# Performance work log

Measured on AMD Instinct MI355X. Metric: run time of the kernel, lower is better.

The kernel has to match this reference:

```python
import jax, jax.numpy as jnp
import numpy as np
from jax.scipy.linalg import solve_triangular

B, T, D = 2, 8192, 1024
HEAD_DIM = 128
H = D // HEAD_DIM  # 8 heads
C = 64             # chunk size (hard-coded in the torch module)


def setup_inputs() -> dict:
    key = jax.random.key(0)
    k0, k1, k2, k3 = jax.random.split(key, 4)
    scale = 0.02
    return {
        "out": jax.random.normal(k0, (B, T, D), jnp.float32),
        "W_write": jax.random.normal(k1, (D, D), jnp.float32) * scale,   # proj_write.weight (out,in)
        "W_read": jax.random.normal(k2, (D, D), jnp.float32) * scale,    # proj_read.weight
        "W_beta": jax.random.normal(k3, (H, D), jnp.float32) * scale,    # proj_beta.weight
        "decay": jnp.full((H,), 4.6, jnp.float32),                        # decay parameter
    }


def reference(out, W_write, W_read, W_beta, decay):
    Bs, Ts, Ds = out.shape
    d = HEAD_DIM
    Hn = Ds // d
    x = out.astype(jnp.float32)

    # keys: L2-normalized per head (F.normalize, eps=1e-12)
    k = x.reshape(Bs, Ts, Hn, d)
    k = k / jnp.maximum(jnp.linalg.norm(k, axis=-1, keepdims=True), 1e-12)
    k = k.transpose(0, 2, 1, 3)                                   # (B,H,T,d)
    v = (x @ W_write.T).reshape(Bs, Ts, Hn, d).transpose(0, 2, 1, 3)
    beta = jax.nn.sigmoid(x @ W_beta.T).transpose(0, 2, 1)[..., None]  # (B,H,T,1)
    v = v * beta
    k_beta = k * beta

    pad = (-Ts) % C
    if pad:
        pw = ((0, 0), (0, 0), (0, pad), (0, 0))
        k, v, k_beta = (jnp.pad(a, pw) for a in (k, v, k_beta))
    Tp = k.shape[2]
    N = Tp // C

    log_gamma = jnp.log(jax.nn.sigmoid(decay))                     # (H,)
    pos = jnp.arange(C, dtype=jnp.float32)
    cum_decay = (pos + 1.0)[None, :] * log_gamma[:, None]          # (H,C)
    Ldiff = cum_decay[:, :, None] - cum_decay[:, None, :]
    L = jnp.tril(jnp.exp(jnp.tril(Ldiff)))                         # (H,C,C)
    decay_exp = jnp.exp(cum_decay)[None, :, None, :, None]         # (1,H,1,C,1)
    chunk_total_decay = jnp.exp(cum_decay[:, -1])[None, :, None, None]  # (1,H,1,1)
    dw = jnp.exp(cum_decay[:, -1:] - cum_decay)[None, :, :, None]  # (1,H,C,1)
    de = jnp.exp(cum_decay)[None, :, :, None]                      # (1,H,C,1)

    k = k.reshape(Bs, Hn, N, C, d)
    v = v.reshape(Bs, Hn, N, C, d)
    k_beta = k_beta.reshape(Bs, Hn, N, C, d)

    # UT transform: original loop computes A = (I - A0)^{-1} with A0 strictly lower
    A0 = jnp.tril(-(jnp.einsum('bhnid,bhnjd->bhnij', k_beta, k) * L[None, :, None]), -1)
    eye = jnp.eye(C, dtype=jnp.float32)
    M = eye - A0                                                    # unit-diag lower triangular
    A = solve_triangular(M, jnp.broadcast_to(eye, M.shape), lower=True, unit_diagonal=True)

    v = A @ v
    k_cumdecay = A @ (k_beta * decay_exp)

    # inter-chunk sequential recurrence over N chunks
    kc = k.transpose(2, 0, 1, 3, 4)            # (N,B,H,C,d)
    vc = v.transpose(2, 0, 1, 3, 4)
    kcd = k_cumdecay.transpose(2, 0, 1, 3, 4)

    def step(S, inp):
        k_i, v_i, kcd_i = inp                  # (B,H,C,d)
        attn = jnp.tril(jnp.einsum('bhid,bhjd->bhij', k_i, k_i) * L[None])
        v_new = v_i - kcd_i @ S
        o_i = (k_i * de) @ S + attn @ v_new
        S_new = chunk_total_decay * S + jnp.einsum('bhcd,bhce->bhde', k_i * dw, v_new)
        return S_new, o_i

    S0 = jnp.zeros((Bs, Hn, d, d), jnp.float32)
    _, o = jax.lax.scan(step, S0, (kc, vc, kcd))  # o: (N,B,H,C,d)

    o = o.transpose(1, 2, 0, 3, 4).reshape(Bs, Hn, Tp, d)
    o = o.transpose(0, 2, 1, 3).reshape(Bs, Tp, Ds)[:, :Ts]
    return out + (o @ W_read.T).astype(out.dtype)
```

## Files before the change

kernel.cpp:

```cpp
#include <hip/hip_runtime.h>
#include <stdint.h>

#define DEV static __device__ __forceinline__

typedef float          f32x4  __attribute__((ext_vector_type(4)));
typedef short          bf16x8 __attribute__((ext_vector_type(8)));
typedef unsigned short u16x4  __attribute__((ext_vector_type(4)));
typedef unsigned short u16x8  __attribute__((ext_vector_type(8)));

#define B_   2
#define T_   8192
#define D_   1024
#define H_   8
#define HD_  128
#define N_   128

DEV float dot4(const float4& a, const float4& b) {
    return a.x * b.x + a.y * b.y + a.z * b.z + a.w * b.w;
}
DEV unsigned short f2bf(float f) {
    union { float f; unsigned u; } v; v.f = f;
    unsigned r = (v.u + 0x7fffu + ((v.u >> 16) & 1u)) >> 16;
    return (unsigned short)r;
}
DEV float bf2f(unsigned short u) {
    union { unsigned u; float f; } v; v.u = ((unsigned)u) << 16;
    return v.f;
}
DEV unsigned pk2(unsigned short h, unsigned short l) {
    return (unsigned)h | ((unsigned)l << 16);
}
DEV bf16x8 mk8(unsigned a, unsigned b, unsigned c, unsigned d) {
    union { unsigned u[4]; bf16x8 v; } t;
    t.u[0] = a; t.u[1] = b; t.u[2] = c; t.u[3] = d;
    return t.v;
}
DEV void cvt4(const float4 v, u16x4* h, u16x4* l) {
    const float* p = (const float*)&v;
    #pragma unroll
    for (int i = 0; i < 4; ++i) {
        unsigned short hv = f2bf(p[i]);
        (*h)[i] = hv;
        (*l)[i] = f2bf(p[i] - bf2f(hv));
    }
}
DEV int swzu(int c, int u) { return u ^ (((c & 7) << 2) | ((c >> 3) & 3)); }

DEV float4* r512(char* base, int r, int u) {
    return (float4*)(base + (r << 9) + ((u << 4) ^ ((r & 7) << 4)));
}

__launch_bounds__(256)
__global__ void prep_kernel(const float* __restrict__ X, const float* __restrict__ Wb,
                            unsigned short* __restrict__ khi, unsigned short* __restrict__ klo,
                            float* __restrict__ beta) {
    int bt = blockIdx.x;
    int b = bt >> 13, t = bt & 8191;
    __shared__ float xrow[D_];
    const float* xp = X + (size_t)bt * D_;
    for (int i = threadIdx.x; i < D_; i += 256) xrow[i] = xp[i];
    __syncthreads();
    int w = threadIdx.x >> 6, lane = threadIdx.x & 63;
    for (int h = w; h < H_; h += 4) {
        const float* xh = xrow + h * HD_;
        float a0 = xh[lane], a1 = xh[lane + 64];
        float s = a0 * a0 + a1 * a1;
        #pragma unroll
        for (int off = 32; off > 0; off >>= 1) s += __shfl_xor(s, off);
        float rn = 1.0f / fmaxf(sqrtf(s), 1e-12f);
        const float* wbh = Wb + (size_t)h * D_;
        float bs = 0.f;
        for (int i = lane; i < D_; i += 64) bs += xrow[i] * wbh[i];
        #pragma unroll
        for (int off = 32; off > 0; off >>= 1) bs += __shfl_xor(bs, off);
        float bet = 1.0f / (1.0f + expf(-bs));
        size_t kbase = ((size_t)(b * H_ + h) * T_ + t) * HD_;
        float x0 = a0 * rn, x1 = a1 * rn;
        unsigned short h0 = f2bf(x0), h1 = f2bf(x1);
        khi[kbase + lane]      = h0;
        khi[kbase + lane + 64] = h1;
        klo[kbase + lane]      = f2bf(x0 - bf2f(h0));
        klo[kbase + lane + 64] = f2bf(x1 - bf2f(h1));
        if (lane == 0) beta[(size_t)(b * H_ + h) * T_ + t] = bet;
    }
}

__launch_bounds__(256, 2)
__global__ void vproj_kernel(const float* __restrict__ X, const float* __restrict__ W,
                             const float* __restrict__ beta, float* __restrict__ vb) {
    extern __shared__ char gs[];
    char* AH = gs;
    char* AL = gs + 16384;
    char* BH = gs + 32768;
    char* BL = gs + 49152;
    int bm = blockIdx.x, bn = blockIdx.y;
    int tid = threadIdx.x;
    int w = tid >> 6, lr = tid & 15, lk = (tid & 63) >> 4;
    int wm = w >> 1, wn = w & 1;

    f32x4 acc[4][4];
    #pragma unroll
    for (int i = 0; i < 4; ++i)
        #pragma unroll
        for (int j = 0; j < 4; ++j) acc[i][j] = (f32x4){0.f, 0.f, 0.f, 0.f};

    for (int kt = 0; kt < 16; ++kt) {
        __syncthreads();
        #pragma unroll
        for (int q = 0; q < 8; ++q) {
            int f = tid + q * 256;
            int row = f >> 4, kq = f & 15;
            float4 av = *(const float4*)(X + (size_t)(bm * 128 + row) * D_ + kt * 64 + kq * 4);
            float4 bv = *(const float4*)(W + (size_t)(bn * 128 + row) * D_ + kt * 64 + kq * 4);
            u16x4 ah, al, bh, bl;
            cvt4(av, &ah, &al);
            cvt4(bv, &bh, &bl);
            int off = row * 128 + ((((kq >> 1) ^ (row & 7))) << 4) + ((kq & 1) << 3);
            *(u16x4*)(AH + off) = ah; *(u16x4*)(AL + off) = al;
            *(u16x4*)(BH + off) = bh; *(u16x4*)(BL + off) = bl;
        }
        __syncthreads();
        #pragma unroll
        for (int ks = 0; ks < 2; ++ks) {
            bf16x8 aH[4], aL[4], bH[4], bL[4];
            #pragma unroll
            for (int mt = 0; mt < 4; ++mt) {
                int row = wm * 64 + mt * 16 + lr;
                int off = row * 128 + (((ks * 4 + lk) ^ (row & 7)) << 4);
                aH[mt] = *(const bf16x8*)(AH + off);
                aL[mt] = *(const bf16x8*)(AL + off);
            }
            #pragma unroll
            for (int nt = 0; nt < 4; ++nt) {
                int row = wn * 64 + nt * 16 + lr;
                int off = row * 128 + (((ks * 4 + lk) ^ (row & 7)) << 4);
                bH[nt] = *(const bf16x8*)(BH + off);
                bL[nt] = *(const bf16x8*)(BL + off);
            }
            #pragma unroll
            for (int mt = 0; mt < 4; ++mt)
                #pragma unroll
                for (int nt = 0; nt < 4; ++nt) {
                    acc[mt][nt] = __builtin_amdgcn_mfma_f32_16x16x32_bf16(aH[mt], bH[nt], acc[mt][nt], 0, 0, 0);
                    acc[mt][nt] = __builtin_amdgcn_mfma_f32_16x16x32_bf16(aH[mt], bL[nt], acc[mt][nt], 0, 0, 0);
                    acc[mt][nt] = __builtin_amdgcn_mfma_f32_16x16x32_bf16(aL[mt], bH[nt], acc[mt][nt], 0, 0, 0);
                }
        }
    }
    #pragma unroll
    for (int mt = 0; mt < 4; ++mt)
        #pragma unroll
        for (int r = 0; r < 4; ++r) {
            int m = bm * 128 + wm * 64 + mt * 16 + lk * 4 + r;
            int b = m >> 13, t = m & 8191;
            float bet = beta[(size_t)(b * H_ + bn) * T_ + t];
            size_t ob = ((size_t)(b * H_ + bn) * T_ + t) * HD_;
            #pragma unroll
            for (int nt = 0; nt < 4; ++nt)
                vb[ob + wn * 64 + nt * 16 + lr] = acc[mt][nt][r] * bet;
        }
}

__launch_bounds__(256, 2)
__global__ void chunk_kernel(const unsigned short* __restrict__ khi,
                             const unsigned short* __restrict__ klo,
                             float* __restrict__ vb,
                             const float* __restrict__ beta_g,
                             const float* __restrict__ decay,
                             unsigned short* __restrict__ attn_g,
                             unsigned short* __restrict__ kcdhi_g,
                             unsigned short* __restrict__ kcdlo_g) {
    extern __shared__ char cs[];
    char*  sk = cs;
    float* sa = (float*)(cs + 32768);
    float* sm = (float*)(cs + 49152);
    __shared__ float sb[64];
    __shared__ float swgt[64];

    int cid = blockIdx.x;
    int bh = cid >> 7, cn = cid & 127;
    int h = bh & 7;
    int tid = threadIdx.x;
    float dec = decay[h];
    float sg = 1.0f / (1.0f + expf(-dec));
    float lg = logf(sg);
    size_t base = (size_t)cid * 8192;

    #pragma unroll
    for (int lq = 0; lq < 4; ++lq) {
        int f = tid + lq * 256;
        int c = f >> 4, u0 = (f & 15) << 1;
        u16x8 hh = *(const u16x8*)(khi + base + (size_t)f * 8);
        u16x8 ll = *(const u16x8*)(klo + base + (size_t)f * 8);
        float4 v0 = {bf2f(hh[0]) + bf2f(ll[0]), bf2f(hh[1]) + bf2f(ll[1]),
                     bf2f(hh[2]) + bf2f(ll[2]), bf2f(hh[3]) + bf2f(ll[3])};
        float4 v1 = {bf2f(hh[4]) + bf2f(ll[4]), bf2f(hh[5]) + bf2f(ll[5]),
                     bf2f(hh[6]) + bf2f(ll[6]), bf2f(hh[7]) + bf2f(ll[7])};
        *r512(sk, c, u0)     = v0;
        *r512(sk, c, u0 + 1) = v1;
    }
    if (tid < 64) {
        float bv = beta_g[(size_t)bh * T_ + cn * 64 + tid];
        sb[tid] = bv;
        swgt[tid] = bv * expf((float)(tid + 1) * lg);
    }
    __syncthreads();

    int bi = tid >> 4, bj = tid & 15;
    float dacc[4][4] = {};
    for (int u = 0; u < 32; ++u) {
        float4 ka[4], kc[4];
        #pragma unroll
        for (int i = 0; i < 4; ++i) ka[i] = *r512(sk, bi * 4 + i, u);
        #pragma unroll
        for (int j = 0; j < 4; ++j) kc[j] = *r512(sk, bj + 16 * j, u);
        #pragma unroll
        for (int i = 0; i < 4; ++i)
            #pragma unroll
            for (int j = 0; j < 4; ++j)
                dacc[i][j] += dot4(ka[i], kc[j]);
    }
    size_t abase = (size_t)cid * 4096;
    #pragma unroll
    for (int i = 0; i < 4; ++i) {
        int gi = bi * 4 + i;
        #pragma unroll
        for (int j = 0; j < 4; ++j) {
            int gj = bj + 16 * j;
            float dv = dacc[i][j];
            float dfac = expf((float)(gi - gj) * lg);
            attn_g[abase + (size_t)gi * 64 + gj] = (gi >= gj) ? f2bf(dv * dfac) : (unsigned short)0;
            sm[gi * 64 + gj] = (gj < gi) ? sb[gi] * dv * dfac : ((gi == gj) ? 1.f : 0.f);
        }
    }
    __syncthreads();

    if (tid < 64) {
        int j = tid;
        for (int i = 0; i < j; ++i) sa[i * 64 + j] = 0.f;
        sa[j * 64 + j] = 1.f;
        for (int i = j + 1; i < 64; ++i) {
            float s = 0.f;
            for (int p = j; p < i; ++p) s += sm[i * 64 + p] * sa[p * 64 + j];
            sa[i * 64 + j] = -s;
        }
    }
    __syncthreads();

    int ti = tid >> 4, te = tid & 15;
    {
        float ko[4][8] = {};
        for (int p = 0; p < 64; ++p) {
            float w = swgt[p];
            float4 k0 = *r512(sk, p, te * 2);
            float4 k1 = *r512(sk, p, te * 2 + 1);
            float kv[8] = {k0.x, k0.y, k0.z, k0.w, k1.x, k1.y, k1.z, k1.w};
            float a0 = sa[(ti * 4 + 0) * 64 + p] * w;
            float a1 = sa[(ti * 4 + 1) * 64 + p] * w;
            float a2 = sa[(ti * 4 + 2) * 64 + p] * w;
            float a3 = sa[(ti * 4 + 3) * 64 + p] * w;
            #pragma unroll
            for (int e = 0; e < 8; ++e) {
                ko[0][e] = fmaf(a0, kv[e], ko[0][e]);
                ko[1][e] = fmaf(a1, kv[e], ko[1][e]);
                ko[2][e] = fmaf(a2, kv[e], ko[2][e]);
                ko[3][e] = fmaf(a3, kv[e], ko[3][e]);
            }
        }
        #pragma unroll
        for (int i = 0; i < 4; ++i) {
            u16x8 hh, ll;
            #pragma unroll
            for (int e = 0; e < 8; ++e) {
                float t = -ko[i][e];
                unsigned short hv = f2bf(t);
                hh[e] = hv;
                ll[e] = f2bf(t - bf2f(hv));
            }
            size_t off = base + (size_t)(ti * 4 + i) * 128 + te * 8;
            *(u16x8*)(kcdhi_g + off) = hh;
            *(u16x8*)(kcdlo_g + off) = ll;
        }
    }
    __syncthreads();

    #pragma unroll
    for (int lq = 0; lq < 8; ++lq) {
        int f = tid + lq * 256;
        int r = f >> 5, u = f & 31;
        *r512(sk, r, u) = ((const float4*)(vb + base))[f];
    }
    __syncthreads();

    {
        float vo[4][8] = {};
        for (int p = 0; p < 64; ++p) {
            float4 v0 = *r512(sk, p, te * 2);
            float4 v1 = *r512(sk, p, te * 2 + 1);
            float vv[8] = {v0.x, v0.y, v0.z, v0.w, v1.x, v1.y, v1.z, v1.w};
            float a0 = sa[(ti * 4 + 0) * 64 + p];
            float a1 = sa[(ti * 4 + 1) * 64 + p];
            float a2 = sa[(ti * 4 + 2) * 64 + p];
            float a3 = sa[(ti * 4 + 3) * 64 + p];
            #pragma unroll
            for (int e = 0; e < 8; ++e) {
                vo[0][e] = fmaf(a0, vv[e], vo[0][e]);
                vo[1][e] = fmaf(a1, vv[e], vo[1][e]);
                vo[2][e] = fmaf(a2, vv[e], vo[2][e]);
                vo[3][e] = fmaf(a3, vv[e], vo[3][e]);
            }
        }
        #pragma unroll
        for (int i = 0; i < 4; ++i) {
            float4 lo = {vo[i][0], vo[i][1], vo[i][2], vo[i][3]};
            float4 hi = {vo[i][4], vo[i][5], vo[i][6], vo[i][7]};
            size_t off = base + (size_t)(ti * 4 + i) * 128 + te * 8;
            *(float4*)(vb + off)     = lo;
            *(float4*)(vb + off + 4) = hi;
        }
    }
}

__launch_bounds__(512, 1)
__global__ void scan_kernel(const unsigned short* __restrict__ khi,
                            const unsigned short* __restrict__ klo,
                            const float* __restrict__ vpr,
                            const unsigned short* __restrict__ kcdhi,
                            const unsigned short* __restrict__ kcdlo,
                            const unsigned short* __restrict__ att,
                            const float* __restrict__ decay,
                            unsigned short* __restrict__ obuf) {
    extern __shared__ char ls[];
    char* KP = ls;
    char* SH = ls + 65536;
    char* SL = ls + 69632;
    char* VH = ls + 73728;
    char* VL = ls + 75776;
    char* WH = ls + 77824;
    char* WL = ls + 79872;

    int bid = blockIdx.x;
    int h7 = bid & 7;
    int strip = (bid >> 3) & 7;
    int bh = ((bid >> 6) << 3) + h7;
    int e0 = strip * 16;
    int tid = threadIdx.x;
    int w = tid >> 6, l = tid & 63, lr = l & 15, lk = l >> 4;
    int grp = w >> 2, cw = w & 3;
    float dec = decay[bh & 7];
    float sg = 1.0f / (1.0f + expf(-dec));
    float lg = logf(sg);
    float g64 = expf(64.f * lg);
    float dev4[4], gw4[4];
    #pragma unroll
    for (int r = 0; r < 4; ++r) {
        int c = cw * 16 + lk * 4 + r;
        dev4[r] = expf((float)(c + 1) * lg);
        gw4[r]  = expf((float)(63 - c) * lg);
    }

    f32x4 Sacc = (f32x4){0.f, 0.f, 0.f, 0.f};

    unsigned sh_[4][4], sl_[4][4];
    bf16x8 fH[4], fL[4];
    bf16x8 atA[2];
    f32x4 vnA;

    {
        size_t nb = (size_t)bh * N_ * 8192;
        size_t na = (size_t)bh * N_ * 4096;
        #pragma unroll
        for (int q = 0; q < 4; ++q) {
            int idx = tid + q * 512;
            u16x4 hh = *(const u16x4*)(khi + nb + (size_t)idx * 4);
            u16x4 ll = *(const u16x4*)(klo + nb + (size_t)idx * 4);
            #pragma unroll
            for (int j = 0; j < 4; ++j) { sh_[q][j] = hh[j]; sl_[q][j] = ll[j]; }
        }
        if (grp == 0) {
            #pragma unroll
            for (int ks = 0; ks < 4; ++ks) {
                size_t off = nb + (size_t)(cw * 16 + lr) * 128 + ks * 32 + lk * 8;
                fH[ks] = *(const bf16x8*)(kcdhi + off);
                fL[ks] = *(const bf16x8*)(kcdlo + off);
            }
            #pragma unroll
            for (int r = 0; r < 4; ++r)
                vnA[r] = vpr[nb + (size_t)(cw * 16 + lk * 4 + r) * 128 + e0 + lr];
        } else {
            #pragma unroll
            for (int ks = 0; ks < 4; ++ks) {
                size_t off = nb + (size_t)(cw * 16 + lr) * 128 + ks * 32 + lk * 8;
                fH[ks] = *(const bf16x8*)(khi + off);
                fL[ks] = *(const bf16x8*)(klo + off);
            }
            #pragma unroll
            for (int ks2 = 0; ks2 < 2; ++ks2)
                atA[ks2] = *(const bf16x8*)(att + na + (size_t)(cw * 16 + lr) * 64 + ks2 * 32 + lk * 8);
        }
        #pragma unroll
        for (int q = 0; q < 4; ++q) {
            int idx = tid + q * 512;
            int c = idx >> 5, un = idx & 31;
            uint4 pkd = {pk2((unsigned short)sh_[q][0], (unsigned short)sl_[q][0]),
                         pk2((unsigned short)sh_[q][1], (unsigned short)sl_[q][1]),
                         pk2((unsigned short)sh_[q][2], (unsigned short)sl_[q][2]),
                         pk2((unsigned short)sh_[q][3], (unsigned short)sl_[q][3])};
            *(uint4*)(KP + c * 512 + (swzu(c, un) << 4)) = pkd;
        }
    }

    for (int cn = 0; cn < N_; ++cn) {
        const char* KPc = KP + (cn & 1) * 32768;

        {
            u16x4 h4, l4;
            #pragma unroll
            for (int r = 0; r < 4; ++r) {
                unsigned short hv = f2bf(Sacc[r]);
                h4[r] = hv;
                l4[r] = f2bf(Sacc[r] - bf2f(hv));
            }
            int unit = 2 * w + (lk >> 1);
            int off = lr * 256 + ((unit ^ (lr & 7)) << 4) + ((lk & 1) << 3);
            *(u16x4*)(SH + off) = h4;
            *(u16x4*)(SL + off) = l4;
        }
        __syncthreads();

        bf16x8 BH[4], BL[4];
        #pragma unroll
        for (int ks = 0; ks < 4; ++ks) {
            int off = lr * 256 + (((ks * 4 + lk) ^ (lr & 7)) << 4);
            BH[ks] = *(const bf16x8*)(SH + off);
            BL[ks] = *(const bf16x8*)(SL + off);
        }
        f32x4 acc1, acc2;
        if (grp == 0) {
            acc1 = vnA; acc2 = (f32x4){0.f, 0.f, 0.f, 0.f};
            __builtin_amdgcn_s_setprio(1);
            #pragma unroll
            for (int ks = 0; ks < 2; ++ks) {
                acc1 = __builtin_amdgcn_mfma_f32_16x16x32_bf16(fH[ks], BH[ks], acc1, 0, 0, 0);
                acc2 = __builtin_amdgcn_mfma_f32_16x16x32_bf16(fH[ks+2], BH[ks+2], acc2, 0, 0, 0);
                acc1 = __builtin_amdgcn_mfma_f32_16x16x32_bf16(fH[ks], BL[ks], acc1, 0, 0, 0);
                acc2 = __builtin_amdgcn_mfma_f32_16x16x32_bf16(fH[ks+2], BL[ks+2], acc2, 0, 0, 0);
                acc1 = __builtin_amdgcn_mfma_f32_16x16x32_bf16(fL[ks], BH[ks], acc1, 0, 0, 0);
                acc2 = __builtin_amdgcn_mfma_f32_16x16x32_bf16(fL[ks+2], BH[ks+2], acc2, 0, 0, 0);
            }
            __builtin_amdgcn_s_setprio(0);
            u16x4 h4, l4, wh4, wl4;
            #pragma unroll
            for (int r = 0; r < 4; ++r) {
                float vv = acc1[r] + acc2[r];
                unsigned short hv = f2bf(vv);
                h4[r] = hv; l4[r] = f2bf(vv - bf2f(hv));
                float wv = vv * gw4[r];
                unsigned short wh = f2bf(wv);
                wh4[r] = wh; wl4[r] = f2bf(wv - bf2f(wh));
            }
            int cu = 2 * cw + (lk >> 1);
            int off = lr * 128 + ((cu ^ (lr & 7)) << 4) + ((lk & 1) << 3);
            *(u16x4*)(VH + off) = h4;  *(u16x4*)(VL + off) = l4;
            *(u16x4*)(WH + off) = wh4; *(u16x4*)(WL + off) = wl4;
        } else {
            acc1 = (f32x4){0.f, 0.f, 0.f, 0.f}; acc2 = acc1;
            __builtin_amdgcn_s_setprio(1);
            #pragma unroll
            for (int ks = 0; ks < 2; ++ks) {
                acc1 = __builtin_amdgcn_mfma_f32_16x16x32_bf16(fH[ks], BH[ks], acc1, 0, 0, 0);
                acc2 = __builtin_amdgcn_mfma_f32_16x16x32_bf16(fH[ks+2], BH[ks+2], acc2, 0, 0, 0);
                acc1 = __builtin_amdgcn_mfma_f32_16x16x32_bf16(fH[ks], BL[ks], acc1, 0, 0, 0);
                acc2 = __builtin_amdgcn_mfma_f32_16x16x32_bf16(fH[ks+2], BL[ks+2], acc2, 0, 0, 0);
                acc1 = __builtin_amdgcn_mfma_f32_16x16x32_bf16(fL[ks], BH[ks], acc1, 0, 0, 0);
                acc2 = __builtin_amdgcn_mfma_f32_16x16x32_bf16(fL[ks+2], BH[ks+2], acc2, 0, 0, 0);
            }
            __builtin_amdgcn_s_setprio(0);
        }
        __syncthreads();

        bf16x8 WHf[2], WLf[2];
        #pragma unroll
        for (int ks2 = 0; ks2 < 2; ++ks2) {
            int off = lr * 128 + (((ks2 * 4 + lk) ^ (lr & 7)) << 4);
            WHf[ks2] = *(const bf16x8*)(WH + off);
            WLf[ks2] = *(const bf16x8*)(WL + off);
        }
        if (grp == 1) {
            bf16x8 VHf[2], VLf[2];
            #pragma unroll
            for (int ks2 = 0; ks2 < 2; ++ks2) {
                int off = lr * 128 + (((ks2 * 4 + lk) ^ (lr & 7)) << 4);
                VHf[ks2] = *(const bf16x8*)(VH + off);
                VLf[ks2] = *(const bf16x8*)(VL + off);
            }
            f32x4 om;
            #pragma unroll
            for (int r = 0; r < 4; ++r) om[r] = (acc1[r] + acc2[r]) * dev4[r];
            #pragma unroll
            for (int ks2 = 0; ks2 < 2; ++ks2) {
                om = __builtin_amdgcn_mfma_f32_16x16x32_bf16(atA[ks2], VHf[ks2], om, 0, 0, 0);
                om = __builtin_amdgcn_mfma_f32_16x16x32_bf16(atA[ks2], VLf[ks2], om, 0, 0, 0);
            }
            size_t ob = ((size_t)bh * T_ + (size_t)cn * 64) * 128 + e0 + lr;
            #pragma unroll
            for (int r = 0; r < 4; ++r)
                obuf[ob + (size_t)(cw * 16 + lk * 4 + r) * 128] = f2bf(om[r]);
        }

        if (cn + 1 < N_) {
            size_t nb = ((size_t)bh * N_ + cn + 1) * 8192;
            size_t na = ((size_t)bh * N_ + cn + 1) * 4096;
            #pragma unroll
            for (int q = 0; q < 4; ++q) {
                int idx = tid + q * 512;
                u16x4 hh = *(const u16x4*)(khi + nb + (size_t)idx * 4);
                u16x4 ll = *(const u16x4*)(klo + nb + (size_t)idx * 4);
                #pragma unroll
                for (int j = 0; j < 4; ++j) { sh_[q][j] = hh[j]; sl_[q][j] = ll[j]; }
            }
            if (grp == 0) {
                #pragma unroll
                for (int ks = 0; ks < 4; ++ks) {
                    size_t off = nb + (size_t)(cw * 16 + lr) * 128 + ks * 32 + lk * 8;
                    fH[ks] = *(const bf16x8*)(kcdhi + off);
                    fL[ks] = *(const bf16x8*)(kcdlo + off);
                }
                #pragma unroll
                for (int r = 0; r < 4; ++r)
                    vnA[r] = vpr[nb + (size_t)(cw * 16 + lk * 4 + r) * 128 + e0 + lr];
            } else {
                #pragma unroll
                for (int ks = 0; ks < 4; ++ks) {
                    size_t off = nb + (size_t)(cw * 16 + lr) * 128 + ks * 32 + lk * 8;
                    fH[ks] = *(const bf16x8*)(khi + off);
                    fL[ks] = *(const bf16x8*)(klo + off);
                }
                #pragma unroll
                for (int ks2 = 0; ks2 < 2; ++ks2)
                    atA[ks2] = *(const bf16x8*)(att + na + (size_t)(cw * 16 + lr) * 64 + ks2 * 32 + lk * 8);
            }
        }

        {
            #pragma unroll
            for (int r = 0; r < 4; ++r) Sacc[r] *= g64;
            int dk = w * 16 + lr;
            int du = dk >> 2, db = (dk & 3) << 2;
            bf16x8 tH[2], tL[2];
            #pragma unroll
            for (int ks2 = 0; ks2 < 2; ++ks2) {
                unsigned uv[8];
                #pragma unroll
                for (int j = 0; j < 8; ++j) {
                    int c = ks2 * 32 + lk * 8 + j;
                    uv[j] = *(const unsigned*)(KPc + c * 512 + (swzu(c, du) << 4) + db);
                }
                tH[ks2] = mk8((uv[0] & 0xffffu) | (uv[1] << 16), (uv[2] & 0xffffu) | (uv[3] << 16),
                              (uv[4] & 0xffffu) | (uv[5] << 16), (uv[6] & 0xffffu) | (uv[7] << 16));
                tL[ks2] = mk8((uv[0] >> 16) | (uv[1] & 0xffff0000u), (uv[2] >> 16) | (uv[3] & 0xffff0000u),
                              (uv[4] >> 16) | (uv[5] & 0xffff0000u), (uv[6] >> 16) | (uv[7] & 0xffff0000u));
            }
            f32x4 tmp = (f32x4){0.f, 0.f, 0.f, 0.f};
            __builtin_amdgcn_s_setprio(1);
            Sacc = __builtin_amdgcn_mfma_f32_16x16x32_bf16(tH[0], WHf[0], Sacc, 0, 0, 0);
            tmp  = __builtin_amdgcn_mfma_f32_16x16x32_bf16(tH[1], WHf[1], tmp,  0, 0, 0);
            Sacc = __builtin_amdgcn_mfma_f32_16x16x32_bf16(tH[0], WLf[0], Sacc, 0, 0, 0);
            tmp  = __builtin_amdgcn_mfma_f32_16x16x32_bf16(tH[1], WLf[1], tmp,  0, 0, 0);
            Sacc = __builtin_amdgcn_mfma_f32_16x16x32_bf16(tL[0], WHf[0], Sacc, 0, 0, 0);
            tmp  = __builtin_amdgcn_mfma_f32_16x16x32_bf16(tL[1], WHf[1], tmp,  0, 0, 0);
            __builtin_amdgcn_s_setprio(0);
            #pragma unroll
            for (int r = 0; r < 4; ++r) Sacc[r] += tmp[r];
        }

        if (cn + 1 < N_) {
            char* KPn = KP + ((cn + 1) & 1) * 32768;
            #pragma unroll
            for (int q = 0; q < 4; ++q) {
                int idx = tid + q * 512;
                int c = idx >> 5, un = idx & 31;
                uint4 pkd = {pk2((unsigned short)sh_[q][0], (unsigned short)sl_[q][0]),
                             pk2((unsigned short)sh_[q][1], (unsigned short)sl_[q][1]),
                             pk2((unsigned short)sh_[q][2], (unsigned short)sl_[q][2]),
                             pk2((unsigned short)sh_[q][3], (unsigned short)sl_[q][3])};
                *(uint4*)(KPn + c * 512 + (swzu(c, un) << 4)) = pkd;
            }
        }
    }
}

__launch_bounds__(256, 2)
__global__ void final_kernel(const float* __restrict__ X, const float* __restrict__ W,
                             const unsigned short* __restrict__ OB, float* __restrict__ out) {
    extern __shared__ char gs[];
    char* AO = gs;
    char* BH = gs + 16384;
    char* BL = gs + 32768;
    int bm = blockIdx.x, bn = blockIdx.y;
    int tid = threadIdx.x;
    int w = tid >> 6, lr = tid & 15, lk = (tid & 63) >> 4;
    int wm = w >> 1, wn = w & 1;

    f32x4 acc[4][4];
    #pragma unroll
    for (int i = 0; i < 4; ++i)
        #pragma unroll
        for (int j = 0; j < 4; ++j) acc[i][j] = (f32x4){0.f, 0.f, 0.f, 0.f};

    for (int kt = 0; kt < 16; ++kt) {
        int hh = kt >> 1, e0g = (kt & 1) * 64;
        __syncthreads();
        #pragma unroll
        for (int q = 0; q < 4; ++q) {
            int f = tid + q * 256;
            int row = f >> 3, un = f & 7;
            int m = bm * 128 + row;
            int b = m >> 13, t = m & 8191;
            u16x8 av = *(const u16x8*)(OB + (((size_t)(b * H_ + hh) * T_ + t) << 7) + e0g + un * 8);
            int off = row * 128 + ((un ^ (row & 7)) << 4);
            *(u16x8*)(AO + off) = av;
        }
        #pragma unroll
        for (int q = 0; q < 8; ++q) {
            int f = tid + q * 256;
            int row = f >> 4, kq = f & 15;
            float4 bv = *(const float4*)(W + (size_t)(bn * 128 + row) * D_ + kt * 64 + kq * 4);
            u16x4 bh, bl;
            cvt4(bv, &bh, &bl);
            int off = row * 128 + ((((kq >> 1) ^ (row & 7))) << 4) + ((kq & 1) << 3);
            *(u16x4*)(BH + off) = bh; *(u16x4*)(BL + off) = bl;
        }
        __syncthreads();
        #pragma unroll
        for (int ks = 0; ks < 2; ++ks) {
            bf16x8 aO[4], bH[4], bL[4];
            #pragma unroll
            for (int mt = 0; mt < 4; ++mt) {
                int row = wm * 64 + mt * 16 + lr;
                int off = row * 128 + (((ks * 4 + lk) ^ (row & 7)) << 4);
                aO[mt] = *(const bf16x8*)(AO + off);
            }
            #pragma unroll
            for (int nt = 0; nt < 4; ++nt) {
                int row = wn * 64 + nt * 16 + lr;
                int off = row * 128 + (((ks * 4 + lk) ^ (row & 7)) << 4);
                bH[nt] = *(const bf16x8*)(BH + off);
                bL[nt] = *(const bf16x8*)(BL + off);
            }
            #pragma unroll
            for (int mt = 0; mt < 4; ++mt)
                #pragma unroll
                for (int nt = 0; nt < 4; ++nt) {
                    acc[mt][nt] = __builtin_amdgcn_mfma_f32_16x16x32_bf16(aO[mt], bH[nt], acc[mt][nt], 0, 0, 0);
                    acc[mt][nt] = __builtin_amdgcn_mfma_f32_16x16x32_bf16(aO[mt], bL[nt], acc[mt][nt], 0, 0, 0);
                }
        }
    }
    #pragma unroll
    for (int mt = 0; mt < 4; ++mt)
        #pragma unroll
        for (int r = 0; r < 4; ++r) {
            int m = bm * 128 + wm * 64 + mt * 16 + lk * 4 + r;
            size_t xo = (size_t)m * D_ + bn * 128;
            #pragma unroll
            for (int nt = 0; nt < 4; ++nt) {
                int n = wn * 64 + nt * 16 + lr;
                out[xo + n] = X[xo + n] + acc[mt][nt][r];
            }
        }
}

extern "C" void kernel_launch(void* const* d_in, const int* in_sizes, int n_in,
                              void* d_out, int out_size, void* d_ws, size_t ws_size,
                              hipStream_t stream) {
    const float* X   = (const float*)d_in[0];
    const float* Ww  = (const float*)d_in[1];
    const float* Wr  = (const float*)d_in[2];
    const float* Wb  = (const float*)d_in[3];
    const float* dec = (const float*)d_in[4];

    char* ws = (char*)d_ws;
    unsigned short* khi  = (unsigned short*)(ws);
    unsigned short* klo  = (unsigned short*)(ws + 33554432);
    float*          vb   = (float*)(ws + 67108864);
    unsigned short* kcdh = (unsigned short*)(ws + 134217728);
    unsigned short* kcdl = (unsigned short*)(ws + 167772160);
    unsigned short* attn = (unsigned short*)(ws + 201326592);
    float*          beta = (float*)(ws + 218103808);
    unsigned short* obuf = (unsigned short*)(ws + 218628096);
    if (ws_size < 252182528ull) return;

    hipFuncSetAttribute((const void*)vproj_kernel, hipFuncAttributeMaxDynamicSharedMemorySize, 65536);
    hipFuncSetAttribute((const void*)chunk_kernel, hipFuncAttributeMaxDynamicSharedMemorySize, 65536);
    hipFuncSetAttribute((const void*)scan_kernel,  hipFuncAttributeMaxDynamicSharedMemorySize, 81920);
    hipFuncSetAttribute((const void*)final_kernel, hipFuncAttributeMaxDynamicSharedMemorySize, 49152);

    hipLaunchKernelGGL(prep_kernel, dim3(B_ * T_), dim3(256), 0, stream, X, Wb, khi, klo, beta);
    hipLaunchKernelGGL(vproj_kernel, dim3(128, 8), dim3(256), 65536, stream, X, Ww, beta, vb);
    hipLaunchKernelGGL(chunk_kernel, dim3(B_ * H_ * N_), dim3(256), 65536, stream,
                       khi, klo, vb, beta, dec, attn, kcdh, kcdl);
    hipLaunchKernelGGL(scan_kernel, dim3(128), dim3(512), 81920, stream,
                       khi, klo, vb, kcdh, kcdl, attn, dec, obuf);
    hipLaunchKernelGGL(final_kernel, dim3(128, 8), dim3(256), 49152, stream, X, Wr, obuf, (float*)d_out);
}
```

Before: 1.152 ms.

## Precompute decay-weighted transposed keys in chunk kernel, simplify scan state update

The chunk kernel now writes a transposed, decay-weighted copy of k (k*dw) as bf16 hi/lo split, so the sequential scan loads it directly instead of staging k into LDS each step and transposing it. The scan no longer forms a decay-weighted v and uses plain v_new for the state update. Its output is written in fp32 into the v buffer, and the final projection splits it into hi/lo bf16 with an extra MFMA. The lo part of the new buffer, and its MFMA in the state update, are used only when the workspace is large enough; otherwise state-update precision drops. The change adds chunk-kernel work and memory traffic to shorten the serial critical path in the scan.

```diff
diff --git a/kernel.cpp b/kernel.cpp
--- a/kernel.cpp
+++ b/kernel.cpp
@@ -27,14 +27,6 @@
     union { unsigned u; float f; } v; v.u = ((unsigned)u) << 16;
     return v.f;
 }
-DEV unsigned pk2(unsigned short h, unsigned short l) {
-    return (unsigned)h | ((unsigned)l << 16);
-}
-DEV bf16x8 mk8(unsigned a, unsigned b, unsigned c, unsigned d) {
-    union { unsigned u[4]; bf16x8 v; } t;
-    t.u[0] = a; t.u[1] = b; t.u[2] = c; t.u[3] = d;
-    return t.v;
-}
 DEV void cvt4(const float4 v, u16x4* h, u16x4* l) {
     const float* p = (const float*)&v;
     #pragma unroll
@@ -44,10 +36,11 @@
         (*l)[i] = f2bf(p[i] - bf2f(hv));
     }
 }
-DEV int swzu(int c, int u) { return u ^ (((c & 7) << 2) | ((c >> 3) & 3)); }
-
 DEV float4* r512(char* base, int r, int u) {
     return (float4*)(base + (r << 9) + ((u << 4) ^ ((r & 7) << 4)));
+}
+DEV float ld_sk(char* base, int c, int dk) {
+    return *(float*)(base + (c << 9) + ((((dk >> 2) << 4) ^ ((c & 7) << 4)) + ((dk & 3) << 2)));
 }
 
 __launch_bounds__(256)
@@ -169,7 +162,9 @@
                              const float* __restrict__ decay,
                              unsigned short* __restrict__ attn_g,
                              unsigned short* __restrict__ kcdhi_g,
-                             unsigned short* __restrict__ kcdlo_g) {
+                             unsigned short* __restrict__ kcdlo_g,
+                             unsigned short* __restrict__ kdwh_g,
+                             unsigned short* __restrict__ kdwl_g) {
     extern __shared__ char cs[];
     char*  sk = cs;
     float* sa = (float*)(cs + 32768);
@@ -282,6 +277,25 @@
             *(u16x8*)(kcdlo_g + off) = ll;
         }
     }
+
+    {
+        int dk = tid >> 1, ch = (tid & 1) * 32;
+        #pragma unroll
+        for (int q = 0; q < 4; ++q) {
+            u16x8 th, tl;
+            #pragma unroll
+            for (int j = 0; j < 8; ++j) {
+                int c = ch + q * 8 + j;
+                float kv = ld_sk(sk, c, dk) * expf((float)(63 - c) * lg);
+                unsigned short hv = f2bf(kv);
+                th[j] = hv;
+                tl[j] = f2bf(kv - bf2f(hv));
+            }
+            size_t off = base + (size_t)dk * 64 + ch + q * 8;
+            *(u16x8*)(kdwh_g + off) = th;
+            if (kdwl_g) *(u16x8*)(kdwl_g + off) = tl;
+        }
+    }
     __syncthreads();
 
     #pragma unroll
@@ -324,25 +338,21 @@
 __launch_bounds__(512, 1)
 __global__ void scan_kernel(const unsigned short* __restrict__ khi,
                             const unsigned short* __restrict__ klo,
-                            const float* __restrict__ vpr,
-                            const unsigned short* __restrict__ kcdhi,
-                            const unsigned short* __restrict__ kcdlo,
+                            float* __restrict__ vb,
+                            const unsigned short* __restrict__ kcdh,
+                            const unsigned short* __restrict__ kcdl,
                             const unsigned short* __restrict__ att,
-                            const float* __restrict__ decay,
-                            unsigned short* __restrict__ obuf) {
-    extern __shared__ char ls[];
-    char* KP = ls;
-    char* SH = ls + 65536;
-    char* SL = ls + 69632;
-    char* VH = ls + 73728;
-    char* VL = ls + 75776;
-    char* WH = ls + 77824;
-    char* WL = ls + 79872;
+                            const unsigned short* __restrict__ kdwh,
+                            const unsigned short* __restrict__ kdwl,
+                            const float* __restrict__ decay) {
+    __shared__ char SH[4096];
+    __shared__ char SL[4096];
+    __shared__ char VH[2048];
+    __shared__ char VL[2048];
 
     int bid = blockIdx.x;
-    int h7 = bid & 7;
+    int bh = ((bid >> 6) << 3) + (bid & 7);
     int strip = (bid >> 3) & 7;
-    int bh = ((bid >> 6) << 3) + h7;
     int e0 = strip * 16;
     int tid = threadIdx.x;
     int w = tid >> 6, l = tid & 63, lr = l & 15, lk = l >> 4;
@@ -351,17 +361,14 @@
     float sg = 1.0f / (1.0f + expf(-dec));
     float lg = logf(sg);
     float g64 = expf(64.f * lg);
-    float dev4[4], gw4[4];
-    #pragma unroll
-    for (int r = 0; r < 4; ++r) {
-        int c = cw * 16 + lk * 4 + r;
-        dev4[r] = expf((float)(c + 1) * lg);
-        gw4[r]  = expf((float)(63 - c) * lg);
-    }
+    float dev4[4];
+    #pragma unroll
+    for (int r = 0; r < 4; ++r)
+        dev4[r] = expf((float)(cw * 16 + lk * 4 + r + 1) * lg);
+    const bool haveLo = (kdwl != nullptr);
 
     f32x4 Sacc = (f32x4){0.f, 0.f, 0.f, 0.f};
 
-    unsigned sh_[4][4], sl_[4][4];
     bf16x8 fH[4], fL[4];
     bf16x8 atA[2];
     f32x4 vnA;
@@ -369,24 +376,16 @@
     {
         size_t nb = (size_t)bh * N_ * 8192;
         size_t na = (size_t)bh * N_ * 4096;
-        #pragma unroll
-        for (int q = 0; q < 4; ++q) {
-            int idx = tid + q * 512;
-            u16x4 hh = *(const u16x4*)(khi + nb + (size_t)idx * 4);
-            u16x4 ll = *(const u16x4*)(klo + nb + (size_t)idx * 4);
-            #pragma unroll
-            for (int j = 0; j < 4; ++j) { sh_[q][j] = hh[j]; sl_[q][j] = ll[j]; }
-        }
         if (grp == 0) {
             #pragma unroll
             for (int ks = 0; ks < 4; ++ks) {
                 size_t off = nb + (size_t)(cw * 16 + lr) * 128 + ks * 32 + lk * 8;
-                fH[ks] = *(const bf16x8*)(kcdhi + off);
-                fL[ks] = *(const bf16x8*)(kcdlo + off);
+                fH[ks] = *(const bf16x8*)(kcdh + off);
+                fL[ks] = *(const bf16x8*)(kcdl + off);
             }
             #pragma unroll
             for (int r = 0; r < 4; ++r)
-                vnA[r] = vpr[nb + (size_t)(cw * 16 + lk * 4 + r) * 128 + e0 + lr];
+                vnA[r] = vb[nb + (size_t)(cw * 16 + lk * 4 + r) * 128 + e0 + lr];
         } else {
             #pragma unroll
             for (int ks = 0; ks < 4; ++ks) {
@@ -398,20 +397,10 @@
             for (int ks2 = 0; ks2 < 2; ++ks2)
                 atA[ks2] = *(const bf16x8*)(att + na + (size_t)(cw * 16 + lr) * 64 + ks2 * 32 + lk * 8);
         }
-        #pragma unroll
-        for (int q = 0; q < 4; ++q) {
-            int idx = tid + q * 512;
-            int c = idx >> 5, un = idx & 31;
-            uint4 pkd = {pk2((unsigned short)sh_[q][0], (unsigned short)sl_[q][0]),
-                         pk2((unsigned short)sh_[q][1], (unsigned short)sl_[q][1]),
-                         pk2((unsigned short)sh_[q][2], (unsigned short)sl_[q][2]),
-                         pk2((unsigned short)sh_[q][3], (unsigned short)sl_[q][3])};
-            *(uint4*)(KP + c * 512 + (swzu(c, un) << 4)) = pkd;
-        }
     }
 
     for (int cn = 0; cn < N_; ++cn) {
-        const char* KPc = KP + (cn & 1) * 32768;
+        size_t cb8 = ((size_t)bh * N_ + cn) * 8192;
 
         {
             u16x4 h4, l4;
@@ -449,20 +438,16 @@
                 acc2 = __builtin_amdgcn_mfma_f32_16x16x32_bf16(fL[ks+2], BH[ks+2], acc2, 0, 0, 0);
             }
             __builtin_amdgcn_s_setprio(0);
-            u16x4 h4, l4, wh4, wl4;
+            u16x4 h4, l4;
             #pragma unroll
             for (int r = 0; r < 4; ++r) {
                 float vv = acc1[r] + acc2[r];
                 unsigned short hv = f2bf(vv);
                 h4[r] = hv; l4[r] = f2bf(vv - bf2f(hv));
-                float wv = vv * gw4[r];
-                unsigned short wh = f2bf(wv);
-                wh4[r] = wh; wl4[r] = f2bf(wv - bf2f(wh));
             }
             int cu = 2 * cw + (lk >> 1);
             int off = lr * 128 + ((cu ^ (lr & 7)) << 4) + ((lk & 1) << 3);
             *(u16x4*)(VH + off) = h4;  *(u16x4*)(VL + off) = l4;
-            *(u16x4*)(WH + off) = wh4; *(u16x4*)(WL + off) = wl4;
         } else {
             acc1 = (f32x4){0.f, 0.f, 0.f, 0.f}; acc2 = acc1;
             __builtin_amdgcn_s_setprio(1);
@@ -479,21 +464,21 @@
         }
         __syncthreads();
 
-        bf16x8 WHf[2], WLf[2];
+        bf16x8 VHf[2], VLf[2];
         #pragma unroll
         for (int ks2 = 0; ks2 < 2; ++ks2) {
             int off = lr * 128 + (((ks2 * 4 + lk) ^ (lr & 7)) << 4);
-            WHf[ks2] = *(const bf16x8*)(WH + off);
-            WLf[ks2] = *(const bf16x8*)(WL + off);
+            VHf[ks2] = *(const bf16x8*)(VH + off);
+            VLf[ks2] = *(const bf16x8*)(VL + off);
+        }
+        bf16x8 tH[2], tL[2];
+        #pragma unroll
+        for (int ks2 = 0; ks2 < 2; ++ks2) {
+            size_t off = cb8 + (size_t)(w * 16 + lr) * 64 + ks2 * 32 + lk * 8;
+            tH[ks2] = *(const bf16x8*)(kdwh + off);
+            if (haveLo) tL[ks2] = *(const bf16x8*)(kdwl + off);
         }
         if (grp == 1) {
-            bf16x8 VHf[2], VLf[2];
-            #pragma unroll
-            for (int ks2 = 0; ks2 < 2; ++ks2) {
-                int off = lr * 128 + (((ks2 * 4 + lk) ^ (lr & 7)) << 4);
-                VHf[ks2] = *(const bf16x8*)(VH + off);
-                VLf[ks2] = *(const bf16x8*)(VL + off);
-            }
             f32x4 om;
             #pragma unroll
             for (int r = 0; r < 4; ++r) om[r] = (acc1[r] + acc2[r]) * dev4[r];
@@ -502,33 +487,24 @@
                 om = __builtin_amdgcn_mfma_f32_16x16x32_bf16(atA[ks2], VHf[ks2], om, 0, 0, 0);
                 om = __builtin_amdgcn_mfma_f32_16x16x32_bf16(atA[ks2], VLf[ks2], om, 0, 0, 0);
             }
-            size_t ob = ((size_t)bh * T_ + (size_t)cn * 64) * 128 + e0 + lr;
             #pragma unroll
             for (int r = 0; r < 4; ++r)
-                obuf[ob + (size_t)(cw * 16 + lk * 4 + r) * 128] = f2bf(om[r]);
+                vb[cb8 + (size_t)(cw * 16 + lk * 4 + r) * 128 + e0 + lr] = om[r];
         }
 
         if (cn + 1 < N_) {
             size_t nb = ((size_t)bh * N_ + cn + 1) * 8192;
             size_t na = ((size_t)bh * N_ + cn + 1) * 4096;
-            #pragma unroll
-            for (int q = 0; q < 4; ++q) {
-                int idx = tid + q * 512;
-                u16x4 hh = *(const u16x4*)(khi + nb + (size_t)idx * 4);
-                u16x4 ll = *(const u16x4*)(klo + nb + (size_t)idx * 4);
-                #pragma unroll
-                for (int j = 0; j < 4; ++j) { sh_[q][j] = hh[j]; sl_[q][j] = ll[j]; }
-            }
             if (grp == 0) {
                 #pragma unroll
                 for (int ks = 0; ks < 4; ++ks) {
                     size_t off = nb + (size_t)(cw * 16 + lr) * 128 + ks * 32 + lk * 8;
-                    fH[ks] = *(const bf16x8*)(kcdhi + off);
-                    fL[ks] = *(const bf16x8*)(kcdlo + off);
+                    fH[ks] = *(const bf16x8*)(kcdh + off);
+                    fL[ks] = *(const bf16x8*)(kcdl + off);
                 }
                 #pragma unroll
                 for (int r = 0; r < 4; ++r)
-                    vnA[r] = vpr[nb + (size_t)(cw * 16 + lk * 4 + r) * 128 + e0 + lr];
+                    vnA[r] = vb[nb + (size_t)(cw * 16 + lk * 4 + r) * 128 + e0 + lr];
             } else {
                 #pragma unroll
                 for (int ks = 0; ks < 4; ++ks) {
@@ -545,58 +521,31 @@
         {
             #pragma unroll
             for (int r = 0; r < 4; ++r) Sacc[r] *= g64;
-            int dk = w * 16 + lr;
-            int du = dk >> 2, db = (dk & 3) << 2;
-            bf16x8 tH[2], tL[2];
-            #pragma unroll
-            for (int ks2 = 0; ks2 < 2; ++ks2) {
-                unsigned uv[8];
-                #pragma unroll
-                for (int j = 0; j < 8; ++j) {
-                    int c = ks2 * 32 + lk * 8 + j;
-                    uv[j] = *(const unsigned*)(KPc + c * 512 + (swzu(c, du) << 4) + db);
-                }
-                tH[ks2] = mk8((uv[0] & 0xffffu) | (uv[1] << 16), (uv[2] & 0xffffu) | (uv[3] << 16),
-                              (uv[4] & 0xffffu) | (uv[5] << 16), (uv[6] & 0xffffu) | (uv[7] << 16));
-                tL[ks2] = mk8((uv[0] >> 16) | (uv[1] & 0xffff0000u), (uv[2] >> 16) | (uv[3] & 0xffff0000u),
-                              (uv[4] >> 16) | (uv[5] & 0xffff0000u), (uv[6] >> 16) | (uv[7] & 0xffff0000u));
-            }
             f32x4 tmp = (f32x4){0.f, 0.f, 0.f, 0.f};
             __builtin_amdgcn_s_setprio(1);
-            Sacc = __builtin_amdgcn_mfma_f32_16x16x32_bf16(tH[0], WHf[0], Sacc, 0, 0, 0);
-            tmp  = __builtin_amdgcn_mfma_f32_16x16x32_bf16(tH[1], WHf[1], tmp,  0, 0, 0);
-            Sacc = __builtin_amdgcn_mfma_f32_16x16x32_bf16(tH[0], WLf[0], Sacc, 0, 0, 0);
-            tmp  = __builtin_amdgcn_mfma_f32_16x16x32_bf16(tH[1], WLf[1], tmp,  0, 0, 0);
-            Sacc = __builtin_amdgcn_mfma_f32_16x16x32_bf16(tL[0], WHf[0], Sacc, 0, 0, 0);
-            tmp  = __builtin_amdgcn_mfma_f32_16x16x32_bf16(tL[1], WHf[1], tmp,  0, 0, 0);
+            Sacc = __builtin_amdgcn_mfma_f32_16x16x32_bf16(tH[0], VHf[0], Sacc, 0, 0, 0);
+            tmp  = __builtin_amdgcn_mfma_f32_16x16x32_bf16(tH[1], VHf[1], tmp,  0, 0, 0);
+            Sacc = __builtin_amdgcn_mfma_f32_16x16x32_bf16(tH[0], VLf[0], Sacc, 0, 0, 0);
+            tmp  = __builtin_amdgcn_mfma_f32_16x16x32_bf16(tH[1], VLf[1], tmp,  0, 0, 0);
+            if (haveLo) {
+                Sacc = __builtin_amdgcn_mfma_f32_16x16x32_bf16(tL[0], VHf[0], Sacc, 0, 0, 0);
+                tmp  = __builtin_amdgcn_mfma_f32_16x16x32_bf16(tL[1], VHf[1], tmp,  0, 0, 0);
+            }
             __builtin_amdgcn_s_setprio(0);
             #pragma unroll
             for (int r = 0; r < 4; ++r) Sacc[r] += tmp[r];
-        }
-
-        if (cn + 1 < N_) {
-            char* KPn = KP + ((cn + 1) & 1) * 32768;
-            #pragma unroll
-            for (int q = 0; q < 4; ++q) {
-                int idx = tid + q * 512;
-                int c = idx >> 5, un = idx & 31;
-                uint4 pkd = {pk2((unsigned short)sh_[q][0], (unsigned short)sl_[q][0]),
-                             pk2((unsigned short)sh_[q][1], (unsigned short)sl_[q][1]),
-                             pk2((unsigned short)sh_[q][2], (unsigned short)sl_[q][2]),
-                             pk2((unsigned short)sh_[q][3], (unsigned short)sl_[q][3])};
-                *(uint4*)(KPn + c * 512 + (swzu(c, un) << 4)) = pkd;
-            }
         }
     }
 }
 
 __launch_bounds__(256, 2)
 __global__ void final_kernel(const float* __restrict__ X, const float* __restrict__ W,
-                             const unsigned short* __restrict__ OB, float* __restrict__ out) {
+                             const float* __restrict__ OB, float* __restrict__ out) {
     extern __shared__ char gs[];
-    char* AO = gs;
-    char* BH = gs + 16384;
-    char* BL = gs + 32768;
+    char* AH = gs;
+    char* AL = gs + 16384;
+    char* BH = gs + 32768;
+    char* BL = gs + 49152;
     int bm = blockIdx.x, bn = blockIdx.y;
     int tid = threadIdx.x;
     int w = tid >> 6, lr = tid & 15, lk = (tid & 63) >> 4;
@@ -612,34 +561,30 @@
         int hh = kt >> 1, e0g = (kt & 1) * 64;
         __syncthreads();
         #pragma unroll
-        for (int q = 0; q < 4; ++q) {
-            int f = tid + q * 256;
-            int row = f >> 3, un = f & 7;
-            int m = bm * 128 + row;
-            int b = m >> 13, t = m & 8191;
-            u16x8 av = *(const u16x8*)(OB + (((size_t)(b * H_ + hh) * T_ + t) << 7) + e0g + un * 8);
-            int off = row * 128 + ((un ^ (row & 7)) << 4);
-            *(u16x8*)(AO + off) = av;
-        }
-        #pragma unroll
         for (int q = 0; q < 8; ++q) {
             int f = tid + q * 256;
             int row = f >> 4, kq = f & 15;
+            int m = bm * 128 + row;
+            int b = m >> 13, t = m & 8191;
+            float4 av = *(const float4*)(OB + (((size_t)(b * H_ + hh) * T_ + t) << 7) + e0g + kq * 4);
             float4 bv = *(const float4*)(W + (size_t)(bn * 128 + row) * D_ + kt * 64 + kq * 4);
-            u16x4 bh, bl;
+            u16x4 ah, al, bh, bl;
+            cvt4(av, &ah, &al);
             cvt4(bv, &bh, &bl);
             int off = row * 128 + ((((kq >> 1) ^ (row & 7))) << 4) + ((kq & 1) << 3);
+            *(u16x4*)(AH + off) = ah; *(u16x4*)(AL + off) = al;
             *(u16x4*)(BH + off) = bh; *(u16x4*)(BL + off) = bl;
         }
         __syncthreads();
         #pragma unroll
         for (int ks = 0; ks < 2; ++ks) {
-            bf16x8 aO[4], bH[4], bL[4];
+            bf16x8 aH[4], aL[4], bH[4], bL[4];
             #pragma unroll
             for (int mt = 0; mt < 4; ++mt) {
                 int row = wm * 64 + mt * 16 + lr;
                 int off = row * 128 + (((ks * 4 + lk) ^ (row & 7)) << 4);
-                aO[mt] = *(const bf16x8*)(AO + off);
+                aH[mt] = *(const bf16x8*)(AH + off);
+                aL[mt] = *(const bf16x8*)(AL + off);
             }
             #pragma unroll
             for (int nt = 0; nt < 4; ++nt) {
@@ -652,8 +597,9 @@
             for (int mt = 0; mt < 4; ++mt)
                 #pragma unroll
                 for (int nt = 0; nt < 4; ++nt) {
-                    acc[mt][nt] = __builtin_amdgcn_mfma_f32_16x16x32_bf16(aO[mt], bH[nt], acc[mt][nt], 0, 0, 0);
-                    acc[mt][nt] = __builtin_amdgcn_mfma_f32_16x16x32_bf16(aO[mt], bL[nt], acc[mt][nt], 0, 0, 0);
+                    acc[mt][nt] = __builtin_amdgcn_mfma_f32_16x16x32_bf16(aH[mt], bH[nt], acc[mt][nt], 0, 0, 0);
+                    acc[mt][nt] = __builtin_amdgcn_mfma_f32_16x16x32_bf16(aH[mt], bL[nt], acc[mt][nt], 0, 0, 0);
+                    acc[mt][nt] = __builtin_amdgcn_mfma_f32_16x16x32_bf16(aL[mt], bH[nt], acc[mt][nt], 0, 0, 0);
                 }
         }
     }
@@ -688,19 +634,21 @@
     unsigned short* kcdl = (unsigned short*)(ws + 167772160);
     unsigned short* attn = (unsigned short*)(ws + 201326592);
     float*          beta = (float*)(ws + 218103808);
-    unsigned short* obuf = (unsigned short*)(ws + 218628096);
+    unsigned short* kdwh = (unsigned short*)(ws + 218628096);
+    unsigned short* kdwl = (ws_size >= 285736960ull)
+                         ? (unsigned short*)(ws + 252182528)
+                         : (unsigned short*)nullptr;
     if (ws_size < 252182528ull) return;
 
     hipFuncSetAttribute((const void*)vproj_kernel, hipFuncAttributeMaxDynamicSharedMemorySize, 65536);
     hipFuncSetAttribute((const void*)chunk_kernel, hipFuncAttributeMaxDynamicSharedMemorySize, 65536);
-    hipFuncSetAttribute((const void*)scan_kernel,  hipFuncAttributeMaxDynamicSharedMemorySize, 81920);
-    hipFuncSetAttribute((const void*)final_kernel, hipFuncAttributeMaxDynamicSharedMemorySize, 49152);
+    hipFuncSetAttribute((const void*)final_kernel, hipFuncAttributeMaxDynamicSharedMemorySize, 65536);
 
     hipLaunchKernelGGL(prep_kernel, dim3(B_ * T_), dim3(256), 0, stream, X, Wb, khi, klo, beta);
     hipLaunchKernelGGL(vproj_kernel, dim3(128, 8), dim3(256), 65536, stream, X, Ww, beta, vb);
     hipLaunchKernelGGL(chunk_kernel, dim3(B_ * H_ * N_), dim3(256), 65536, stream,
-                       khi, klo, vb, beta, dec, attn, kcdh, kcdl);
-    hipLaunchKernelGGL(scan_kernel, dim3(128), dim3(512), 81920, stream,
-                       khi, klo, vb, kcdh, kcdl, attn, dec, obuf);
-    hipLaunchKernelGGL(final_kernel, dim3(128, 8), dim3(256), 49152, stream, X, Wr, obuf, (float*)d_out);
-}
+                       khi, klo, vb, beta, dec, attn, kcdh, kcdl, kdwh, kdwl);
+    hipLaunchKernelGGL(scan_kernel, dim3(128), dim3(512), 0, stream,
+                       khi, klo, vb, kcdh, kcdl, attn, kdwh, kdwl, dec);
+    hipLaunchKernelGGL(final_kernel, dim3(128, 8), dim3(256), 65536, stream, X, Wr, vb, (float*)d_out);
+}
```

New measurement: 1.085 ms. 5.9% less time.
